# Optimization experiments

Measured on AMD Instinct MI355X. Metric: run time of the kernel, lower is better.

## Reference

```python
import jax, jax.numpy as jnp
import numpy as np


def setup_inputs() -> dict:
    key = jax.random.key(0)
    ks = jax.random.split(key, 7)
    N = 262144
    Ka, La = 8, 8
    Kb, Lb, Mb = 8, 8, 4
    Kc, Lc, Mc = 8, 8, 4
    return {
        "x": jax.random.normal(ks[0], (N, 2), dtype=jnp.float32),
        "a_real": 0.001 * jax.random.normal(ks[1], (Ka, La), dtype=jnp.float32),
        "a_imag": 0.001 * jax.random.normal(ks[2], (Ka, La), dtype=jnp.float32),
        "b_real": 0.001 * jax.random.normal(ks[3], (Kb, Lb, Mb), dtype=jnp.float32),
        "b_imag": 0.001 * jax.random.normal(ks[4], (Kb, Lb, Mb), dtype=jnp.float32),
        "c_real": 0.001 * jax.random.normal(ks[5], (Kc, Lc, Mc), dtype=jnp.float32),
        "c_imag": 0.001 * jax.random.normal(ks[6], (Kc, Lc, Mc), dtype=jnp.float32),
    }


def _gmp(x, a_real, a_imag, b_real, b_imag, c_real, c_imag):
    # x: (N,2) real I/Q -> complex signal (iq_handler equivalent)
    xc = (x[:, 0] + 1j * x[:, 1]).astype(jnp.complex64)
    a = (a_real + 1j * a_imag).astype(jnp.complex64)   # (Ka,La)
    b = (b_real + 1j * b_imag).astype(jnp.complex64)   # (Kb,Lb,Mb)
    c = (c_real + 1j * c_imag).astype(jnp.complex64)   # (Kc,Lc,Mc)
    N = xc.shape[0]
    Ka, La = a.shape
    Kb, Lb, Mb = b.shape
    Kc, Lc, Mc = c.shape
    n = jnp.arange(N)

    # ---- aligned term (a): delayed taps, power series in |x[n-l]| ----
    idx_La = jnp.clip(n[None, :] - jnp.arange(La)[:, None], 0, N - 1)   # (La,N)
    x_La = xc[idx_La]                                                   # (La,N)
    pow_a = jnp.abs(x_La)[..., None] ** jnp.arange(Ka, dtype=jnp.float32)  # (La,N,Ka)
    term_a = jnp.einsum('kl,ln,lnk->n', a, x_La, pow_a)

    # ---- lagging cross-term (b): envelope delayed by extra m >= 0 ----
    idx_Lb = jnp.clip(n[None, :] - jnp.arange(Lb)[:, None], 0, N - 1)   # (Lb,N)
    x_Lb = xc[idx_Lb]                                                   # (Lb,N)
    idx_Mb = jnp.clip(n[None, None, :] - jnp.arange(Lb)[:, None, None]
                      - jnp.arange(Mb)[None, :, None], 0, N - 1)        # (Lb,Mb,N)
    x_Mb = xc[idx_Mb]                                                   # (Lb,Mb,N)
    pow_b = jnp.abs(x_Mb)[..., None] ** jnp.arange(Kb, dtype=jnp.float32)  # (Lb,Mb,N,Kb)
    term_b = jnp.einsum('klm,ln,lmnk->n', b, x_Lb, pow_b)

    # ---- leading cross-term (c): envelope advanced by m >= 0 ----
    idx_Lc = jnp.clip(n[None, :] - jnp.arange(Lc)[:, None], 0, N - 1)   # (Lc,N)
    x_Lc = xc[idx_Lc]                                                   # (Lc,N)
    idx_Mc = jnp.clip(n[None, None, :] - jnp.arange(Lc)[:, None, None]
                      + jnp.arange(Mc)[None, :, None], 0, N - 1)        # (Lc,Mc,N)
    x_Mc = xc[idx_Mc]                                                   # (Lc,Mc,N)
    pow_c = jnp.abs(x_Mc)[..., None] ** jnp.arange(Kc, dtype=jnp.float32)  # (Lc,Mc,N,Kc)
    term_c = jnp.einsum('klm,ln,lmnk->n', c, x_Lc, pow_c)

    y = term_a + term_b + term_c                                        # (N,) complex
    return jnp.stack([y.real, y.imag], axis=-1)                         # back to I/Q (N,2)


def reference(x, a_real, a_imag, b_real, b_imag, c_real, c_imag):
    return _gmp(x, a_real, a_imag, b_real, b_imag, c_real, c_imag)
```

## Files before the change

kernel.cpp:

```cpp
#include <hip/hip_runtime.h>
#include <type_traits>

typedef float v2f __attribute__((ext_vector_type(2)));

template <typename T>
using cptr = T __attribute__((address_space(4)))*;

constexpr int BLOCK = 256;
constexpr int SPB = 128;
constexpr int HALO_LO = 10;
constexpr int HALO_HI = 3;
constexpr int SIG = SPB + HALO_LO + HALO_HI;

template<int I, int N, typename F>
__device__ __forceinline__ void unroll_for(F&& f) {
    if constexpr (I < N) {
        f(std::integral_constant<int, I>{});
        unroll_for<I + 1, N>(static_cast<F&&>(f));
    }
}

__global__ void prefold_kernel(
    const float* __restrict__ a_re, const float* __restrict__ a_im,
    const float* __restrict__ b_re, const float* __restrict__ b_im,
    const float* __restrict__ c_re, const float* __restrict__ c_im,
    float* __restrict__ w)
{
    int idx = threadIdx.x;
    if (idx >= 448) return;
    int l = idx / 56;
    int rem = idx - l * 56;
    int s = rem >> 3;
    int k = rem & 7;
    int akl = k * 8 + l;
    float re, im;
    if (s == 0) {
        re = a_re[akl] + b_re[akl * 4] + c_re[akl * 4];
        im = a_im[akl] + b_im[akl * 4] + c_im[akl * 4];
    } else if (s <= 3) {
        re = b_re[akl * 4 + s];
        im = b_im[akl * 4 + s];
    } else {
        re = c_re[akl * 4 + (s - 3)];
        im = c_im[akl * 4 + (s - 3)];
    }
    w[idx * 2]     = re;
    w[idx * 2 + 1] = im;
}

__global__ __launch_bounds__(BLOCK) void gmp_kernel(
    const float* __restrict__ x,
    const float* __restrict__ wbuf,
    float* __restrict__ out, int N)
{
    __shared__ float sxr[SIG], sxi[SIG], sab[SIG];
    __shared__ float2 part[4][SPB];

    const int t = threadIdx.x;
    const int n0 = blockIdx.x * SPB;

    const float2* x2 = (const float2*)x;
    for (int j = t; j < SIG; j += BLOCK) {
        int g = n0 - HALO_LO + j;
        g = max(0, min(N - 1, g));
        float2 v = x2[g];
        sxr[j] = v.x;
        sxi[j] = v.y;
        sab[j] = __builtin_amdgcn_sqrtf(fmaf(v.x, v.x, v.y * v.y));
    }
    __syncthreads();

    const int s2 = t & 63;
    const int wv = __builtin_amdgcn_readfirstlane(t >> 6);
    auto cw = (cptr<const float>)(unsigned long long)(wbuf + wv * 224);

    const int rb = 2 * s2 + 6 - 2 * wv;
    float rv[9];
    unroll_for<0, 9>([&](auto I) { rv[I.value] = sab[rb + I.value]; });
    float xvr[3], xvi[3];
    unroll_for<0, 3>([&](auto I) {
        xvr[I.value] = sxr[rb + 3 + I.value];
        xvi[I.value] = sxi[rb + 3 + I.value];
    });

    float y0r = 0.f, y0i = 0.f, y1r = 0.f, y1i = 0.f;

    unroll_for<0, 2>([&](auto LL) {
        constexpr int ll = LL.value;
        v2f S0 = {0.f, 0.f}, S1 = {0.f, 0.f};
        unroll_for<0, 7>([&](auto Sc) {
            constexpr int s = Sc.value;
            constexpr int d = (s == 0) ? 0 : ((s <= 3) ? -s : (s - 3));
            constexpr int off = ll * 112 + s * 16;
            float cre[8], cim[8];
            unroll_for<0, 8>([&](auto K) {
                cre[K.value] = cw[off + 2 * K.value];
                cim[K.value] = cw[off + 2 * K.value + 1];
            });
            const float r0 = rv[4 - ll + d];
            const float r1 = rv[5 - ll + d];
            const v2f rr0 = {r0, r0};
            const v2f rr1 = {r1, r1};
            v2f acc0 = {cre[7], cim[7]};
            v2f acc1 = acc0;
            unroll_for<0, 7>([&](auto Kc) {
                constexpr int k = 6 - Kc.value;
                const v2f wk = {cre[k], cim[k]};
                acc0 = __builtin_elementwise_fma(acc0, rr0, wk);
                acc1 = __builtin_elementwise_fma(acc1, rr1, wk);
            });
            S0 += acc0;
            S1 += acc1;
        });
        {
            const float xre = xvr[1 - ll], xim = xvi[1 - ll];
            y0r = fmaf(xre, S0.x, fmaf(-xim, S0.y, y0r));
            y0i = fmaf(xre, S0.y, fmaf( xim, S0.x, y0i));
        }
        {
            const float xre = xvr[2 - ll], xim = xvi[2 - ll];
            y1r = fmaf(xre, S1.x, fmaf(-xim, S1.y, y1r));
            y1i = fmaf(xre, S1.y, fmaf( xim, S1.x, y1i));
        }
    });

    part[wv][2 * s2]     = make_float2(y0r, y0i);
    part[wv][2 * s2 + 1] = make_float2(y1r, y1i);
    __syncthreads();

    if (t < SPB) {
        float2 p0 = part[0][t];
        float2 p1 = part[1][t];
        float2 p2 = part[2][t];
        float2 p3 = part[3][t];
        float2 r;
        r.x = (p0.x + p1.x) + (p2.x + p3.x);
        r.y = (p0.y + p1.y) + (p2.y + p3.y);
        const int n = n0 + t;
        if (n < N) ((float2*)out)[n] = r;
    }
}

extern "C" void kernel_launch(void* const* d_in, const int* in_sizes, int n_in,
                              void* d_out, int out_size, void* d_ws, size_t ws_size,
                              hipStream_t stream) {
    const float* x    = (const float*)d_in[0];
    const float* a_re = (const float*)d_in[1];
    const float* a_im = (const float*)d_in[2];
    const float* b_re = (const float*)d_in[3];
    const float* b_im = (const float*)d_in[4];
    const float* c_re = (const float*)d_in[5];
    const float* c_im = (const float*)d_in[6];
    float* out = (float*)d_out;
    float* w   = (float*)d_ws;

    int N = in_sizes[0] / 2;
    prefold_kernel<<<1, 448, 0, stream>>>(a_re, a_im, b_re, b_im, c_re, c_im, w);
    int grid = (N + SPB - 1) / SPB;
    gmp_kernel<<<grid, BLOCK, 0, stream>>>(x, w, out, N);
}
```

Baseline: 15.46 us.

## Assign one output sample per thread over all taps, dropping cross-wave reduction

Each thread now computes one output sample across all 8 delay taps instead of 2 samples across 2 taps per wave. This removes the shared-memory partial buffer, the second barrier and the 4-way reduction, and doubles samples per block. The coefficient reads now hit the same address for every thread, so they can go through scalar loads. In exchange, per-thread serial work and register pressure rise (14 envelope values, 8 complex samples) and the grid has half as many blocks. Occupancy is also hinted through launch bounds.

Measured after the change: 23.49 us. 51.9% more time.

```diff
diff --git a/kernel.cpp b/kernel.cpp
--- a/kernel.cpp
+++ b/kernel.cpp
@@ -7,7 +7,7 @@
 using cptr = T __attribute__((address_space(4)))*;
 
 constexpr int BLOCK = 256;
-constexpr int SPB = 128;
+constexpr int SPB = 256;
 constexpr int HALO_LO = 10;
 constexpr int HALO_HI = 3;
 constexpr int SIG = SPB + HALO_LO + HALO_HI;
@@ -48,13 +48,13 @@
     w[idx * 2 + 1] = im;
 }
 
-__global__ __launch_bounds__(BLOCK) void gmp_kernel(
+__global__ __launch_bounds__(BLOCK, 4) void gmp_kernel(
     const float* __restrict__ x,
     const float* __restrict__ wbuf,
     float* __restrict__ out, int N)
 {
-    __shared__ float sxr[SIG], sxi[SIG], sab[SIG];
-    __shared__ float2 part[4][SPB];
+    __shared__ float2 sx[SIG];
+    __shared__ float sab[SIG];
 
     const int t = threadIdx.x;
     const int n0 = blockIdx.x * SPB;
@@ -64,81 +64,53 @@
         int g = n0 - HALO_LO + j;
         g = max(0, min(N - 1, g));
         float2 v = x2[g];
-        sxr[j] = v.x;
-        sxi[j] = v.y;
+        sx[j] = v;
         sab[j] = __builtin_amdgcn_sqrtf(fmaf(v.x, v.x, v.y * v.y));
     }
     __syncthreads();
 
-    const int s2 = t & 63;
-    const int wv = __builtin_amdgcn_readfirstlane(t >> 6);
-    auto cw = (cptr<const float>)(unsigned long long)(wbuf + wv * 224);
+    auto cw = (cptr<const float>)(unsigned long long)wbuf;
 
-    const int rb = 2 * s2 + 6 - 2 * wv;
-    float rv[9];
-    unroll_for<0, 9>([&](auto I) { rv[I.value] = sab[rb + I.value]; });
-    float xvr[3], xvi[3];
-    unroll_for<0, 3>([&](auto I) {
-        xvr[I.value] = sxr[rb + 3 + I.value];
-        xvi[I.value] = sxi[rb + 3 + I.value];
+    float rv[14];
+    unroll_for<0, 14>([&](auto I) { rv[I.value] = sab[t + I.value]; });
+    float xvr[8], xvi[8];
+    unroll_for<0, 8>([&](auto I) {
+        float2 v = sx[t + 3 + I.value];
+        xvr[I.value] = v.x;
+        xvi[I.value] = v.y;
     });
 
-    float y0r = 0.f, y0i = 0.f, y1r = 0.f, y1i = 0.f;
+    float yr = 0.f, yi = 0.f;
 
-    unroll_for<0, 2>([&](auto LL) {
-        constexpr int ll = LL.value;
-        v2f S0 = {0.f, 0.f}, S1 = {0.f, 0.f};
+    unroll_for<0, 8>([&](auto LL) {
+        constexpr int l = LL.value;
+        v2f S = {0.f, 0.f};
         unroll_for<0, 7>([&](auto Sc) {
             constexpr int s = Sc.value;
             constexpr int d = (s == 0) ? 0 : ((s <= 3) ? -s : (s - 3));
-            constexpr int off = ll * 112 + s * 16;
+            constexpr int off = l * 112 + s * 16;
             float cre[8], cim[8];
             unroll_for<0, 8>([&](auto K) {
                 cre[K.value] = cw[off + 2 * K.value];
                 cim[K.value] = cw[off + 2 * K.value + 1];
             });
-            const float r0 = rv[4 - ll + d];
-            const float r1 = rv[5 - ll + d];
-            const v2f rr0 = {r0, r0};
-            const v2f rr1 = {r1, r1};
-            v2f acc0 = {cre[7], cim[7]};
-            v2f acc1 = acc0;
+            const float r = rv[10 - l + d];
+            const v2f rr = {r, r};
+            v2f acc = {cre[7], cim[7]};
             unroll_for<0, 7>([&](auto Kc) {
                 constexpr int k = 6 - Kc.value;
                 const v2f wk = {cre[k], cim[k]};
-                acc0 = __builtin_elementwise_fma(acc0, rr0, wk);
-                acc1 = __builtin_elementwise_fma(acc1, rr1, wk);
+                acc = __builtin_elementwise_fma(acc, rr, wk);
             });
-            S0 += acc0;
-            S1 += acc1;
+            S += acc;
         });
-        {
-            const float xre = xvr[1 - ll], xim = xvi[1 - ll];
-            y0r = fmaf(xre, S0.x, fmaf(-xim, S0.y, y0r));
-            y0i = fmaf(xre, S0.y, fmaf( xim, S0.x, y0i));
-        }
-        {
-            const float xre = xvr[2 - ll], xim = xvi[2 - ll];
-            y1r = fmaf(xre, S1.x, fmaf(-xim, S1.y, y1r));
-            y1i = fmaf(xre, S1.y, fmaf( xim, S1.x, y1i));
-        }
+        const float xre = xvr[7 - l], xim = xvi[7 - l];
+        yr = fmaf(xre, S.x, fmaf(-xim, S.y, yr));
+        yi = fmaf(xre, S.y, fmaf( xim, S.x, yi));
     });
 
-    part[wv][2 * s2]     = make_float2(y0r, y0i);
-    part[wv][2 * s2 + 1] = make_float2(y1r, y1i);
-    __syncthreads();
-
-    if (t < SPB) {
-        float2 p0 = part[0][t];
-        float2 p1 = part[1][t];
-        float2 p2 = part[2][t];
-        float2 p3 = part[3][t];
-        float2 r;
-        r.x = (p0.x + p1.x) + (p2.x + p3.x);
-        r.y = (p0.y + p1.y) + (p2.y + p3.y);
-        const int n = n0 + t;
-        if (n < N) ((float2*)out)[n] = r;
-    }
+    const int n = n0 + t;
+    if (n < N) ((float2*)out)[n] = make_float2(yr, yi);
 }
 
 extern "C" void kernel_launch(void* const* d_in, const int* in_sizes, int n_in,
```
